# Kernel tuning notes

Hardware: AMD Instinct MI355X
Metric: run time of the kernel (lower is better)

## Reference

```python
import jax, jax.numpy as jnp
import numpy as np

BATCH = 10
HID = 128
OUT = 7
MAX_LEN = 2048


def setup_inputs() -> dict:
    key = jax.random.key(0)
    ks = jax.random.split(key, 10)
    h0 = jax.random.normal(ks[0], (1, BATCH, HID), dtype=jnp.float32)
    c0 = jax.random.normal(ks[1], (1, BATCH, HID), dtype=jnp.float32)
    # target is a sequence of one-hot vectors, shape (MAX_LEN+1, 1, OUT)
    tgt_idx = jax.random.randint(ks[2], (MAX_LEN + 1,), 0, OUT)
    target_onehot = jax.nn.one_hot(tgt_idx, OUT, dtype=jnp.float32)[:, None, :]
    # per-step teacher-forcing coin flips (torch.rand(1) < 0.5 externalized)
    tf_mask = jax.random.bernoulli(ks[3], 0.5, (MAX_LEN,))
    # LSTM parameters, torch gate order [i, f, g, o]; k = 1/sqrt(HID) init scale
    k = 1.0 / np.sqrt(HID)
    W_ih = jax.random.uniform(ks[4], (4 * HID, OUT), minval=-k, maxval=k, dtype=jnp.float32)
    W_hh = jax.random.uniform(ks[5], (4 * HID, HID), minval=-k, maxval=k, dtype=jnp.float32)
    b_ih = jax.random.uniform(ks[6], (4 * HID,), minval=-k, maxval=k, dtype=jnp.float32)
    b_hh = jax.random.uniform(ks[7], (4 * HID,), minval=-k, maxval=k, dtype=jnp.float32)
    W_out = jax.random.uniform(ks[8], (OUT, HID), minval=-k, maxval=k, dtype=jnp.float32)
    b_out = jax.random.uniform(ks[9], (OUT,), minval=-k, maxval=k, dtype=jnp.float32)
    return dict(h0=h0, c0=c0, target_onehot=target_onehot, tf_mask=tf_mask,
                W_ih=W_ih, W_hh=W_hh, b_ih=b_ih, b_hh=b_hh, W_out=W_out, b_out=b_out)


def reference(h0, c0, target_onehot, tf_mask, W_ih, W_hh, b_ih, b_hh, W_out, b_out):
    # initial decoder input: one-hot at last class for all 10 batch items
    x0 = jnp.zeros((BATCH, OUT), jnp.float32).at[:, OUT - 1].set(1.0)
    tgt_next = target_onehot[1:MAX_LEN + 1, 0, :]  # (MAX_LEN, OUT), fed at step i
    bias = b_ih + b_hh

    def step(carry, inp):
        h, c, x = carry            # h,c: (B,HID); x: (B,OUT)
        tf, tgt = inp              # tf: scalar bool; tgt: (OUT,)
        xr = jax.nn.relu(x)
        gates = xr @ W_ih.T + h @ W_hh.T + bias          # (B, 4*HID)
        i_g, f_g, g_g, o_g = jnp.split(gates, 4, axis=-1)
        c2 = jax.nn.sigmoid(f_g) * c + jax.nn.sigmoid(i_g) * jnp.tanh(g_g)
        h2 = jax.nn.sigmoid(o_g) * jnp.tanh(c2)
        logits = h2 @ W_out.T + b_out                    # (B, OUT)
        greedy = jax.nn.one_hot(jnp.argmax(logits, axis=-1), OUT, dtype=jnp.float32)
        nxt = jnp.where(tf, jnp.broadcast_to(tgt, (BATCH, OUT)), greedy)
        return (h2, c2, nxt), logits

    (hT, cT, _), logits = jax.lax.scan(
        step, (h0[0], c0[0], x0), (tf_mask, tgt_next))
    logits = jnp.transpose(logits, (1, 0, 2))            # (B, MAX_LEN, OUT)
    log_probs = jax.nn.log_softmax(logits, axis=-1)
    return log_probs, (hT[None], cT[None])
```

## Files before the change

kernel.cpp:

```cpp
#include <hip/hip_runtime.h>
#include <math.h>

#define BATCH 10
#define HID 128
#define OUT 7
#define MAXLEN 2048
#define NG 512
#define NT 512
#define RINGD 512
#define OFF_STATE ((size_t)BATCH * MAXLEN * OUT)

typedef float float2v __attribute__((ext_vector_type(2)));
typedef float float4v __attribute__((ext_vector_type(4)));

__device__ __forceinline__ float sigm_(float x) { return 1.0f / (1.0f + __expf(-x)); }
__device__ __forceinline__ float tanh_(float x) { return 1.0f - 2.0f / (1.0f + __expf(2.0f * x)); }

__device__ __forceinline__ float2v vlo(float4v v) { return __builtin_shufflevector(v, v, 0, 1); }
__device__ __forceinline__ float2v vhi(float4v v) { return __builtin_shufflevector(v, v, 2, 3); }

__device__ __forceinline__ void pk_fma(float2v& acc, float2v w, float2v h) {
    asm("v_pk_fma_f32 %0, %1, %2, %0" : "+v"(acc) : "v"(w), "v"(h));
}

__device__ __forceinline__ float grp8_sum(float v) {
    v += __int_as_float(__builtin_amdgcn_update_dpp(0, __float_as_int(v), 0xB1, 0xF, 0xF, true));
    v += __int_as_float(__builtin_amdgcn_update_dpp(0, __float_as_int(v), 0x4E, 0xF, 0xF, true));
    v += __int_as_float(__builtin_amdgcn_update_dpp(0, __float_as_int(v), 0x141, 0xF, 0xF, true));
    return v;
}

__global__
__attribute__((amdgpu_flat_work_group_size(NT, NT), amdgpu_waves_per_eu(2, 2)))
void decoder_rnn_kernel(const float* __restrict__ h0,
                        const float* __restrict__ c0,
                        const float* __restrict__ tonehot,
                        const void*  __restrict__ tf_raw,
                        const float* __restrict__ Wih,
                        const float* __restrict__ Whh,
                        const float* __restrict__ bih,
                        const float* __restrict__ bhh,
                        const float* __restrict__ Wout,
                        const float* __restrict__ bout,
                        float* __restrict__ out)
{
    __shared__ __align__(16) float h_lds[HID];
    __shared__ __align__(16) float gates_lds[NG];
    __shared__ float wih_eff[OUT * NG];
    __shared__ float ring[RINGD][OUT];
    __shared__ unsigned char tgt8[MAXLEN];
    __shared__ unsigned char tf8[MAXLEN];
    __shared__ int tf_byte_mode;

    const int t     = threadIdx.x;
    const int lane  = t & 63;
    const int wv    = t >> 6;
    const int ksl   = lane & 7;
    const int grp   = lane >> 3;
    const int b     = blockIdx.x;
    const int gbase = wv * 64 + grp * 8;

    unsigned long long whh_a  = (unsigned long long)Whh;
    unsigned long long wout_a = (unsigned long long)Wout;
    asm volatile("" : "+v"(whh_a), "+v"(wout_a));
    const float* whh_p  = (const float*)whh_a;
    const float* wout_p = (const float*)wout_a;

    float4v wq[8][4];
    #pragma unroll
    for (int g = 0; g < 8; g++)
        #pragma unroll
        for (int c = 0; c < 4; c++)
            wq[g][c] = *(const float4v*)&whh_p[(size_t)(gbase + g) * HID + c * 32 + ksl * 4];
    #pragma unroll
    for (int g = 0; g < 8; g++)
        #pragma unroll
        for (int c = 0; c < 4; c++)
            asm volatile("" : "+v"(wq[g][c]));

    float4v lw[4];
    #pragma unroll
    for (int c = 0; c < 4; c++) { float4v z = {0.f, 0.f, 0.f, 0.f}; lw[c] = z; }
    if (wv < 2 && grp < OUT) {
        #pragma unroll
        for (int c = 0; c < 4; c++)
            lw[c] = *(const float4v*)&wout_p[(size_t)grp * HID + c * 32 + ksl * 4];
    }
    #pragma unroll
    for (int c = 0; c < 4; c++)
        asm volatile("" : "+v"(lw[c]));

    float boutr[OUT];
    #pragma unroll
    for (int j = 0; j < OUT; j++) boutr[j] = bout[j];

    for (int idx = t; idx < OUT * NG; idx += NT) {
        int x = idx >> 9, g = idx & (NG - 1);
        wih_eff[idx] = Wih[g * OUT + x] + bih[g] + bhh[g];
    }
    if (t == 0) tf_byte_mode = 0;
    for (int s = t; s < MAXLEN; s += NT) {
        const float* row = tonehot + (size_t)(s + 1) * OUT;
        int idx = 0;
        #pragma unroll
        for (int j = 0; j < OUT; j++) if (row[j] > 0.5f) idx = j;
        tgt8[s] = (unsigned char)idx;
    }
    __syncthreads();
    {
        const unsigned char* tb = (const unsigned char*)tf_raw;
        int mis = 0;
        for (int p = t; p < MAXLEN; p += NT)
            if ((p & 3) && tb[p]) mis = 1;
        if (mis) atomicOr(&tf_byte_mode, 1);
    }
    float c_reg = 0.f, hv = 0.f;
    if (t < HID) {
        hv    = h0[b * HID + t];
        c_reg = c0[b * HID + t];
        h_lds[t] = hv;
    }
    __syncthreads();
    if (tf_byte_mode) {
        const unsigned char* tb = (const unsigned char*)tf_raw;
        for (int s = t; s < MAXLEN; s += NT) tf8[s] = (tb[s] != 0);
    } else {
        const int* ti = (const int*)tf_raw;
        for (int s = t; s < MAXLEN; s += NT) tf8[s] = (ti[s] != 0);
    }
    __syncthreads();

    float* outlp = out + (size_t)b * MAXLEN * OUT;

    for (int s = 0; s < MAXLEN; s++) {
        int tfp = 0, tgp = 0;
        if (s > 0) { tfp = tf8[s - 1]; tgp = tgt8[s - 1]; }

        float wpre0 = 0.f, wpre1 = 0.f, wpre2 = 0.f, wpre3 = 0.f;
        if (t < HID && tfp) {
            const int xo = tgp * NG;
            wpre0 = wih_eff[xo + t];
            wpre1 = wih_eff[xo + 128 + t];
            wpre2 = wih_eff[xo + 256 + t];
            wpre3 = wih_eff[xo + 384 + t];
        }

        float4v hc[4];
        #pragma unroll
        for (int c = 0; c < 4; c++)
            hc[c] = *(const float4v*)&h_lds[c * 32 + ksl * 4];

        float2v acc[8];
        #pragma unroll
        for (int g = 0; g < 8; g++) { float2v z = {0.f, 0.f}; acc[g] = z; }
        #pragma unroll
        for (int c = 0; c < 4; c++) {
            const float2v hlo = vlo(hc[c]), hhi = vhi(hc[c]);
            #pragma unroll
            for (int g = 0; g < 8; g++) {
                pk_fma(acc[g], vlo(wq[g][c]), hlo);
                pk_fma(acc[g], vhi(wq[g][c]), hhi);
            }
        }
        float a[8];
        #pragma unroll
        for (int g = 0; g < 8; g++) a[g] = grp8_sum(acc[g][0] + acc[g][1]);

        float al = 0.f;
        if (wv < 2) {
            float2v la = {0.f, 0.f};
            #pragma unroll
            for (int c = 0; c < 4; c++) {
                pk_fma(la, vlo(lw[c]), vlo(hc[c]));
                pk_fma(la, vhi(lw[c]), vhi(hc[c]));
            }
            al = grp8_sum(la[0] + la[1]);
        }
        if (ksl == 0) {
            float4v g4a, g4b;
            g4a[0] = a[0]; g4a[1] = a[1]; g4a[2] = a[2]; g4a[3] = a[3];
            g4b[0] = a[4]; g4b[1] = a[5]; g4b[2] = a[6]; g4b[3] = a[7];
            *(float4v*)&gates_lds[gbase]     = g4a;
            *(float4v*)&gates_lds[gbase + 4] = g4b;
        }
        __syncthreads();

        if (t < HID) {
            if (s > 0 && wv == 0 && ksl == 0 && grp < OUT)
                ring[(s - 1) & (RINGD - 1)][grp] = al;
            float w0, w1, w2, w3;
            if (tfp) {
                w0 = wpre0; w1 = wpre1; w2 = wpre2; w3 = wpre3;
            } else {
                int xsel = OUT - 1;
                if (s > 0) {
                    float lg[OUT];
                    #pragma unroll
                    for (int j = 0; j < OUT; j++)
                        lg[j] = __int_as_float(__builtin_amdgcn_readlane(__float_as_int(al), 8 * j)) + boutr[j];
                    float bv = lg[0]; int bi = 0;
                    #pragma unroll
                    for (int j = 1; j < OUT; j++) if (lg[j] > bv) { bv = lg[j]; bi = j; }
                    xsel = bi;
                }
                const int xo = xsel * NG;
                w0 = wih_eff[xo + t];
                w1 = wih_eff[xo + 128 + t];
                w2 = wih_eff[xo + 256 + t];
                w3 = wih_eff[xo + 384 + t];
            }
            const float ri = gates_lds[t]           + w0;
            const float rf = gates_lds[HID + t]     + w1;
            const float rg = gates_lds[2 * HID + t] + w2;
            const float ro = gates_lds[3 * HID + t] + w3;
            const float cn = sigm_(rf) * c_reg + sigm_(ri) * tanh_(rg);
            c_reg = cn;
            hv = sigm_(ro) * tanh_(cn);
            h_lds[t] = hv;
        } else if (t >= 256 && (s & 255) == 1 && s > 256) {
            const int step = (s - 257) + (t - 256);
            const int slot = step & (RINGD - 1);
            float v[OUT];
            #pragma unroll
            for (int j = 0; j < OUT; j++) v[j] = ring[slot][j] + boutr[j];
            float mx = v[0];
            #pragma unroll
            for (int j = 1; j < OUT; j++) mx = fmaxf(mx, v[j]);
            float sum = 0.f;
            #pragma unroll
            for (int j = 0; j < OUT; j++) sum += __expf(v[j] - mx);
            const float lse = mx + __logf(sum);
            float* dst = outlp + (size_t)step * OUT;
            #pragma unroll
            for (int j = 0; j < OUT; j++) dst[j] = v[j] - lse;
        }
        __syncthreads();
    }

    if (wv < 2) {
        float2v la = {0.f, 0.f};
        #pragma unroll
        for (int c = 0; c < 4; c++) {
            const float4v h4 = *(const float4v*)&h_lds[c * 32 + ksl * 4];
            pk_fma(la, vlo(lw[c]), vlo(h4));
            pk_fma(la, vhi(lw[c]), vhi(h4));
        }
        const float al = grp8_sum(la[0] + la[1]);
        if (wv == 0 && ksl == 0 && grp < OUT)
            ring[(MAXLEN - 1) & (RINGD - 1)][grp] = al;
    }
    __syncthreads();
    if (t < 256) {
        const int step = (MAXLEN - 256) + t;
        const int slot = step & (RINGD - 1);
        float v[OUT];
        #pragma unroll
        for (int j = 0; j < OUT; j++) v[j] = ring[slot][j] + boutr[j];
        float mx = v[0];
        #pragma unroll
        for (int j = 1; j < OUT; j++) mx = fmaxf(mx, v[j]);
        float sum = 0.f;
        #pragma unroll
        for (int j = 0; j < OUT; j++) sum += __expf(v[j] - mx);
        const float lse = mx + __logf(sum);
        float* dst = outlp + (size_t)step * OUT;
        #pragma unroll
        for (int j = 0; j < OUT; j++) dst[j] = v[j] - lse;
    }
    if (t < HID) {
        out[OFF_STATE + b * HID + t] = hv;
        out[OFF_STATE + BATCH * HID + b * HID + t] = c_reg;
    }
}

extern "C" void kernel_launch(void* const* d_in, const int* in_sizes, int n_in,
                              void* d_out, int out_size, void* d_ws, size_t ws_size,
                              hipStream_t stream) {
    const float* h0    = (const float*)d_in[0];
    const float* c0    = (const float*)d_in[1];
    const float* toh   = (const float*)d_in[2];
    const void*  tfm   = (const void*) d_in[3];
    const float* Wih   = (const float*)d_in[4];
    const float* Whh   = (const float*)d_in[5];
    const float* bih   = (const float*)d_in[6];
    const float* bhh   = (const float*)d_in[7];
    const float* Wout  = (const float*)d_in[8];
    const float* bout  = (const float*)d_in[9];
    float* out = (float*)d_out;

    decoder_rnn_kernel<<<dim3(BATCH), dim3(NT), 0, stream>>>(
        h0, c0, toh, tfm, Wih, Whh, bih, bhh, Wout, bout, out);
}
```

Before: 2.203 ms.

## Move half of W_hh to padded LDS and stream the rest from global

Drops the register-resident W_hh tile (128 floats per thread). The first 64 columns are staged into padded shared memory (stride 65) and the second half is reloaded from global/L2 every step, apparently to relieve register pressure. To make room in LDS, the logits ring buffer shrinks to 256 and the log-softmax flush now runs every 128 steps. Each serial step now carries LDS and global-load latency on its critical path, where the weights used to sit in registers.

```diff
diff --git a/kernel.cpp b/kernel.cpp
--- a/kernel.cpp
+++ b/kernel.cpp
@@ -7,7 +7,8 @@
 #define MAXLEN 2048
 #define NG 512
 #define NT 512
-#define RINGD 512
+#define RINGD 256
+#define WSTRIDE 65
 #define OFF_STATE ((size_t)BATCH * MAXLEN * OUT)
 
 typedef float float2v __attribute__((ext_vector_type(2)));
@@ -44,10 +45,11 @@
                         const float* __restrict__ bout,
                         float* __restrict__ out)
 {
+    __shared__ __align__(16) float wlds[NG * WSTRIDE];
+    __shared__ float wih_eff[OUT * NG];
+    __shared__ float ring[RINGD][OUT];
     __shared__ __align__(16) float h_lds[HID];
     __shared__ __align__(16) float gates_lds[NG];
-    __shared__ float wih_eff[OUT * NG];
-    __shared__ float ring[RINGD][OUT];
     __shared__ unsigned char tgt8[MAXLEN];
     __shared__ unsigned char tf8[MAXLEN];
     __shared__ int tf_byte_mode;
@@ -60,40 +62,23 @@
     const int b     = blockIdx.x;
     const int gbase = wv * 64 + grp * 8;
 
-    unsigned long long whh_a  = (unsigned long long)Whh;
-    unsigned long long wout_a = (unsigned long long)Wout;
-    asm volatile("" : "+v"(whh_a), "+v"(wout_a));
-    const float* whh_p  = (const float*)whh_a;
-    const float* wout_p = (const float*)wout_a;
-
-    float4v wq[8][4];
-    #pragma unroll
-    for (int g = 0; g < 8; g++)
-        #pragma unroll
-        for (int c = 0; c < 4; c++)
-            wq[g][c] = *(const float4v*)&whh_p[(size_t)(gbase + g) * HID + c * 32 + ksl * 4];
-    #pragma unroll
-    for (int g = 0; g < 8; g++)
-        #pragma unroll
-        for (int c = 0; c < 4; c++)
-            asm volatile("" : "+v"(wq[g][c]));
-
     float4v lw[4];
     #pragma unroll
     for (int c = 0; c < 4; c++) { float4v z = {0.f, 0.f, 0.f, 0.f}; lw[c] = z; }
     if (wv < 2 && grp < OUT) {
         #pragma unroll
         for (int c = 0; c < 4; c++)
-            lw[c] = *(const float4v*)&wout_p[(size_t)grp * HID + c * 32 + ksl * 4];
-    }
-    #pragma unroll
-    for (int c = 0; c < 4; c++)
-        asm volatile("" : "+v"(lw[c]));
+            lw[c] = *(const float4v*)&Wout[(size_t)grp * HID + c * 32 + ksl * 4];
+    }
 
     float boutr[OUT];
     #pragma unroll
     for (int j = 0; j < OUT; j++) boutr[j] = bout[j];
 
+    for (int idx = t; idx < NG * 64; idx += NT) {
+        const int g = idx >> 6, k = idx & 63;
+        wlds[g * WSTRIDE + k] = Whh[(size_t)g * HID + k];
+    }
     for (int idx = t; idx < OUT * NG; idx += NT) {
         int x = idx >> 9, g = idx & (NG - 1);
         wih_eff[idx] = Wih[g * OUT + x] + bih[g] + bhh[g];
@@ -145,6 +130,13 @@
             wpre3 = wih_eff[xo + 384 + t];
         }
 
+        float4v wr[8][2];
+        #pragma unroll
+        for (int g = 0; g < 8; g++)
+            #pragma unroll
+            for (int c = 0; c < 2; c++)
+                wr[g][c] = *(const float4v*)&Whh[(size_t)(gbase + g) * HID + 64 + c * 32 + ksl * 4];
+
         float4v hc[4];
         #pragma unroll
         for (int c = 0; c < 4; c++)
@@ -154,13 +146,18 @@
         #pragma unroll
         for (int g = 0; g < 8; g++) { float2v z = {0.f, 0.f}; acc[g] = z; }
         #pragma unroll
-        for (int c = 0; c < 4; c++) {
-            const float2v hlo = vlo(hc[c]), hhi = vhi(hc[c]);
-            #pragma unroll
-            for (int g = 0; g < 8; g++) {
-                pk_fma(acc[g], vlo(wq[g][c]), hlo);
-                pk_fma(acc[g], vhi(wq[g][c]), hhi);
-            }
+        for (int g = 0; g < 8; g++) {
+            const int wb = (gbase + g) * WSTRIDE + ksl * 4;
+            const float4v wl0 = *(const float4v*)&wlds[wb];
+            const float4v wl1 = *(const float4v*)&wlds[wb + 32];
+            pk_fma(acc[g], vlo(wl0), vlo(hc[0]));
+            pk_fma(acc[g], vhi(wl0), vhi(hc[0]));
+            pk_fma(acc[g], vlo(wl1), vlo(hc[1]));
+            pk_fma(acc[g], vhi(wl1), vhi(hc[1]));
+            pk_fma(acc[g], vlo(wr[g][0]), vlo(hc[2]));
+            pk_fma(acc[g], vhi(wr[g][0]), vhi(hc[2]));
+            pk_fma(acc[g], vlo(wr[g][1]), vlo(hc[3]));
+            pk_fma(acc[g], vhi(wr[g][1]), vhi(hc[3]));
         }
         float a[8];
         #pragma unroll
@@ -217,8 +214,8 @@
             c_reg = cn;
             hv = sigm_(ro) * tanh_(cn);
             h_lds[t] = hv;
-        } else if (t >= 256 && (s & 255) == 1 && s > 256) {
-            const int step = (s - 257) + (t - 256);
+        } else if (t >= 256 && t < 384 && (s & 127) == 1 && s > 128) {
+            const int step = (s - 129) + (t - 256);
             const int slot = step & (RINGD - 1);
             float v[OUT];
             #pragma unroll
@@ -250,8 +247,8 @@
             ring[(MAXLEN - 1) & (RINGD - 1)][grp] = al;
     }
     __syncthreads();
-    if (t < 256) {
-        const int step = (MAXLEN - 256) + t;
+    if (t < 128) {
+        const int step = (MAXLEN - 128) + t;
         const int slot = step & (RINGD - 1);
         float v[OUT];
         #pragma unroll
```

Result: slower. 4.181 ms (+89.8%).
